# Optimization experiments

Measured on AMD Instinct MI355X. Metric: run time of the kernel, lower is better.

The kernel has to match this reference:

```python
import jax, jax.numpy as jnp
import numpy as np

S, B, D_IN, D_SRC, D_ALIGN = 2048, 64, 512, 512, 512


def setup_inputs() -> dict:
    key = jax.random.key(0)
    ks = jax.random.split(key, 6)
    scale = 0.1  # matches uniform_(-0.1, 0.1) init magnitude
    return {
        "input": jax.random.normal(ks[0], (1, B, D_IN), dtype=jnp.float32),
        "source_hids": jax.random.normal(ks[1], (S, B, D_SRC), dtype=jnp.float32),
        "encoder_padding_mask": jnp.zeros((S, B), dtype=bool),
        "W1": jax.random.uniform(ks[2], (D_ALIGN, D_IN + D_SRC), jnp.float32, -scale, scale),
        "b1": jax.random.uniform(ks[3], (D_ALIGN,), jnp.float32, -scale, scale),
        "W2": jax.random.uniform(ks[4], (1, D_ALIGN), jnp.float32, -scale, scale),
        "b2": jax.random.uniform(ks[5], (1,), jnp.float32, -scale, scale),
    }


def reference(input, source_hids, encoder_padding_mask, W1, b1, W2, b2):
    # input: [1, B, D_in] broadcast over srclen; source_hids: [S, B, D_src]
    s = source_hids.shape[0]
    x = jnp.broadcast_to(input, (s,) + input.shape[1:])          # [S, B, D_in]
    cat = jnp.concatenate((x, source_hids), axis=-1)             # [S, B, D_in+D_src]
    h = jnp.tanh(jnp.einsum('sbd,ad->sba', cat, W1) + b1)        # [S, B, D_align]
    scores = jnp.einsum('sba,oa->sbo', h, W2)[..., 0] + b2[0]    # [S, B]
    scores = jnp.where(encoder_padding_mask, -jnp.inf, scores)
    attn = jax.nn.softmax(scores, axis=0)                        # softmax over srclen
    ctx = jnp.einsum('sb,sbd->bd', attn, source_hids)            # [B, D_src]
    return ctx, attn
```

## Files before the change

### kernel.cpp

```cpp
#include <hip/hip_runtime.h>
#include <hip/hip_bf16.h>
#include <math.h>

#define S_LEN 2048
#define BATCH 64
#define DDIM 512

typedef __attribute__((ext_vector_type(8))) short bf16x8;
typedef __attribute__((ext_vector_type(4))) float f32x4;
typedef __attribute__((ext_vector_type(4))) unsigned int u32x4;

typedef __attribute__((address_space(1))) const void g_void;
typedef __attribute__((address_space(3))) void l_void;

__device__ __forceinline__ unsigned short f2bf(float f) {
  unsigned int u = __float_as_uint(f);
  u += 0x7fffu + ((u >> 16) & 1u);
  return (unsigned short)(u >> 16);
}

__device__ __forceinline__ float tanh_fast(float x) {
  float e = __builtin_amdgcn_exp2f(x * 2.88539008177793f);
  return 1.0f - 2.0f * __builtin_amdgcn_rcpf(e + 1.0f);
}

__global__ __launch_bounds__(256) void prep_kernel(
    const float* __restrict__ W1, const float* __restrict__ b1,
    const float* __restrict__ input, unsigned short* __restrict__ W1b,
    float* __restrict__ uprime) {
  __shared__ float w1row[1024];
  const int a = blockIdx.x;
  const int t = threadIdx.x;
  float4 v = *(const float4*)(W1 + a * 1024 + t * 4);
  *(float4*)(w1row + t * 4) = v;
  if (t >= 128) {
    ushort4 u;
    u.x = f2bf(v.x); u.y = f2bf(v.y); u.z = f2bf(v.z); u.w = f2bf(v.w);
    *(ushort4*)(W1b + a * 512 + (t * 4 - 512)) = u;
  }
  __syncthreads();
  if (t < BATCH) {
    const float4* inp = (const float4*)(input + t * 512);
    const float4* wr = (const float4*)w1row;
    float acc = b1[a];
#pragma unroll 4
    for (int d = 0; d < 128; ++d) {
      float4 x = inp[d], w = wr[d];
      acc += x.x * w.x + x.y * w.y + x.z * w.z + x.w * w.w;
    }
    uprime[t * 512 + a] = acc;
  }
}

__global__ __launch_bounds__(512, 4) void scores_kernel(
    const float* __restrict__ src, const unsigned short* __restrict__ W1b,
    const float* __restrict__ uprime, const float* __restrict__ W2,
    float* __restrict__ scores_t) {
  __shared__ unsigned short A_sm[64 * 64];
  __shared__ unsigned short B_sm[512 * 64];
  __shared__ float s_lds[BATCH];

  const int t = threadIdx.x;
  const int s = blockIdx.x;
  const int w = t >> 6;
  const int lane = t & 63;
  const int quad = lane >> 4;
  const int l15 = lane & 15;

  if (t < BATCH) s_lds[t] = 0.f;

  f32x4 acc[4][4];
#pragma unroll
  for (int i = 0; i < 4; ++i)
#pragma unroll
    for (int j = 0; j < 4; ++j) acc[i][j] = (f32x4){0.f, 0.f, 0.f, 0.f};

  const float* srcblk = src + (size_t)s * (BATCH * DDIM);
  const int ar = t >> 3, ap = t & 7, ac = ap ^ (ar & 7);
  const float* gA = srcblk + ar * DDIM + ac * 8;
  unsigned short* ldsA = A_sm + ar * 64 + ap * 8;
  const int br = lane >> 3, bp = lane & 7, bc = bp ^ (br & 7);
  const unsigned short* gBl = W1b + br * DDIM + bc * 8;

  for (int k0 = 0; k0 < DDIM; k0 += 64) {
#pragma unroll
    for (int g = 0; g < 8; ++g) {
      const unsigned short* gp = gBl + (g * 64 + w * 8) * DDIM + k0;
      unsigned short* lp = B_sm + (g * 64 + w * 8) * 64;
      __builtin_amdgcn_global_load_lds((g_void*)gp, (l_void*)lp, 16, 0, 0);
    }
    {
      const float4 v0 = *(const float4*)(gA + k0);
      const float4 v1 = *(const float4*)(gA + k0 + 4);
      unsigned x0 = __float_as_uint(v0.x) + 0x8000u;
      unsigned y0 = __float_as_uint(v0.y) + 0x8000u;
      unsigned z0 = __float_as_uint(v0.z) + 0x8000u;
      unsigned w0 = __float_as_uint(v0.w) + 0x8000u;
      unsigned x1 = __float_as_uint(v1.x) + 0x8000u;
      unsigned y1 = __float_as_uint(v1.y) + 0x8000u;
      unsigned z1 = __float_as_uint(v1.z) + 0x8000u;
      unsigned w1 = __float_as_uint(v1.w) + 0x8000u;
      u32x4 o;
      o.x = __builtin_amdgcn_perm(y0, x0, 0x07060302u);
      o.y = __builtin_amdgcn_perm(w0, z0, 0x07060302u);
      o.z = __builtin_amdgcn_perm(y1, x1, 0x07060302u);
      o.w = __builtin_amdgcn_perm(w1, z1, 0x07060302u);
      *(u32x4*)ldsA = o;
    }
    __syncthreads();

#pragma unroll
    for (int ks = 0; ks < 2; ++ks) {
      const int c = ks * 4 + quad;
      bf16x8 af[4], bfr[4];
#pragma unroll
      for (int i = 0; i < 4; ++i) {
        const int r = i * 16 + l15;
        af[i] = *(const bf16x8*)(A_sm + r * 64 + ((c ^ (r & 7)) << 3));
      }
#pragma unroll
      for (int j = 0; j < 4; ++j) {
        const int n = w * 64 + j * 16 + l15;
        bfr[j] = *(const bf16x8*)(B_sm + n * 64 + ((c ^ (n & 7)) << 3));
      }
#pragma unroll
      for (int i = 0; i < 4; ++i)
#pragma unroll
        for (int j = 0; j < 4; ++j)
          acc[i][j] = __builtin_amdgcn_mfma_f32_16x16x32_bf16(af[i], bfr[j], acc[i][j], 0, 0, 0);
    }
    __syncthreads();
  }

  float w2r[4];
#pragma unroll
  for (int j = 0; j < 4; ++j) w2r[j] = W2[w * 64 + j * 16 + l15];

#pragma unroll
  for (int i = 0; i < 4; ++i) {
#pragma unroll
    for (int r = 0; r < 4; ++r) {
      const int b = i * 16 + quad * 4 + r;
      const float* up = uprime + b * 512 + w * 64 + l15;
      float sp = 0.f;
#pragma unroll
      for (int j = 0; j < 4; ++j)
        sp += w2r[j] * tanh_fast(acc[i][j][r] + up[j * 16]);
      sp += __shfl_xor(sp, 1);
      sp += __shfl_xor(sp, 2);
      sp += __shfl_xor(sp, 4);
      sp += __shfl_xor(sp, 8);
      if (l15 == 0) atomicAdd(&s_lds[b], sp);
    }
  }
  __syncthreads();
  if (t < BATCH) scores_t[t * S_LEN + s] = s_lds[t];
}

__global__ __launch_bounds__(256) void softmax_kernel(
    const float* __restrict__ scores_t, const unsigned char* __restrict__ mask,
    float* __restrict__ attn_g, float* __restrict__ attn_t, int write_t) {
  __shared__ float red[256];
  const int b = blockIdx.x, t = threadIdx.x;
  float m = -__builtin_inff();
  float sc[8];
#pragma unroll
  for (int c = 0; c < 8; ++c) {
    const int s = t + c * 256;
    sc[c] = mask[s * BATCH + b] ? -__builtin_inff() : scores_t[b * S_LEN + s];
    m = fmaxf(m, sc[c]);
  }
  red[t] = m;
  __syncthreads();
  for (int off = 128; off; off >>= 1) {
    if (t < off) red[t] = fmaxf(red[t], red[t + off]);
    __syncthreads();
  }
  m = red[0];
  __syncthreads();
  float sum = 0.f;
#pragma unroll
  for (int c = 0; c < 8; ++c) sum += __expf(sc[c] - m);
  red[t] = sum;
  __syncthreads();
  for (int off = 128; off; off >>= 1) {
    if (t < off) red[t] += red[t + off];
    __syncthreads();
  }
  const float inv = 1.f / red[0];
#pragma unroll
  for (int c = 0; c < 8; ++c) {
    const int s = t + c * 256;
    const float p = __expf(sc[c] - m) * inv;
    attn_g[s * BATCH + b] = p;
    if (write_t) attn_t[b * S_LEN + s] = p;
  }
}

__global__ __launch_bounds__(256) void ctx_partial_kernel(
    const float* __restrict__ src, const float* __restrict__ attn_t,
    float* __restrict__ partial) {
  __shared__ float a_lds[64];
  const int c = blockIdx.x;
  const int b = blockIdx.y;
  const int t = threadIdx.x;
  if (t < 64) a_lds[t] = attn_t[b * S_LEN + c * 64 + t];
  __syncthreads();
  const int f4i = t & 127;
  const int sh = t >> 7;
  const float4* base =
      (const float4*)src + ((size_t)(c * 64 + sh * 32) * BATCH + b) * 128 + f4i;
  float4 acc = {0.f, 0.f, 0.f, 0.f};
#pragma unroll 8
  for (int i = 0; i < 32; ++i) {
    const float a = a_lds[sh * 32 + i];
    float4 v = base[(size_t)i * BATCH * 128];
    acc.x += a * v.x; acc.y += a * v.y; acc.z += a * v.z; acc.w += a * v.w;
  }
  ((float4*)partial)[((size_t)(c * 2 + sh) * BATCH + b) * 128 + f4i] = acc;
}

__global__ __launch_bounds__(256) void ctx_reduce_kernel(
    const float* __restrict__ partial, float* __restrict__ ctx) {
  const int b = blockIdx.x, t = threadIdx.x;
  const float2* p = (const float2*)partial + (size_t)b * 256 + t;
  float2 acc = {0.f, 0.f};
#pragma unroll 8
  for (int c2 = 0; c2 < 64; ++c2) {
    float2 v = p[(size_t)c2 * BATCH * 256];
    acc.x += v.x; acc.y += v.y;
  }
  ((float2*)ctx)[b * 256 + t] = acc;
}

__global__ __launch_bounds__(256) void ctx_atomic_kernel(
    const float* __restrict__ src, const float* __restrict__ attn_g,
    float* __restrict__ ctx) {
  __shared__ float a_lds[128];
  const int s0 = blockIdx.x * 128, b = blockIdx.y, t = threadIdx.x;
  if (t < 128) a_lds[t] = attn_g[(s0 + t) * BATCH + b];
  __syncthreads();
  const int f4i = t & 127;
  const int sh = t >> 7;
  const float4* base =
      (const float4*)src + ((size_t)(s0 + sh * 64) * BATCH + b) * 128 + f4i;
  float4 acc = {0.f, 0.f, 0.f, 0.f};
#pragma unroll 8
  for (int i = 0; i < 64; ++i) {
    const float a = a_lds[sh * 64 + i];
    float4 v = base[(size_t)i * BATCH * 128];
    acc.x += a * v.x; acc.y += a * v.y; acc.z += a * v.z; acc.w += a * v.w;
  }
  float* cp = ctx + b * DDIM + f4i * 4;
  atomicAdd(cp + 0, acc.x);
  atomicAdd(cp + 1, acc.y);
  atomicAdd(cp + 2, acc.z);
  atomicAdd(cp + 3, acc.w);
}

extern "C" void kernel_launch(void* const* d_in, const int* in_sizes, int n_in,
                              void* d_out, int out_size, void* d_ws, size_t ws_size,
                              hipStream_t stream) {
  const float* input = (const float*)d_in[0];
  const float* src = (const float*)d_in[1];
  const unsigned char* mask = (const unsigned char*)d_in[2];
  const float* W1 = (const float*)d_in[3];
  const float* b1 = (const float*)d_in[4];
  const float* W2 = (const float*)d_in[5];

  float* ctx = (float*)d_out;
  float* attn = (float*)d_out + BATCH * DDIM;

  unsigned short* W1b = (unsigned short*)d_ws;
  float* uprime = (float*)((char*)d_ws + 512 * 1024);
  float* scores_t = (float*)((char*)d_ws + 640 * 1024);
  float* attn_t = (float*)((char*)d_ws + 1152 * 1024);
  float* partial = (float*)((char*)d_ws + 1664 * 1024);
  const size_t NEED_ATTN_T = 1664 * 1024;
  const size_t NEED_PARTIAL = 1664 * 1024 + (size_t)64 * BATCH * DDIM * 4;
  const int have_attn_t = ws_size >= NEED_ATTN_T;
  const int have_partial = ws_size >= NEED_PARTIAL;

  prep_kernel<<<512, 256, 0, stream>>>(W1, b1, input, W1b, uprime);
  scores_kernel<<<S_LEN, 512, 0, stream>>>(src, W1b, uprime, W2, scores_t);
  softmax_kernel<<<BATCH, 256, 0, stream>>>(scores_t, mask, attn, attn_t,
                                            have_attn_t && have_partial);
  if (have_partial) {
    ctx_partial_kernel<<<dim3(32, BATCH), 256, 0, stream>>>(src, attn_t, partial);
    ctx_reduce_kernel<<<BATCH, 256, 0, stream>>>(partial, ctx);
  } else {
    hipMemsetAsync(ctx, 0, BATCH * DDIM * sizeof(float), stream);
    ctx_atomic_kernel<<<dim3(16, BATCH), 256, 0, stream>>>(src, attn, ctx);
  }
}
```

Measured before the change: 494.1 us.

## Process two source positions per block and double-buffer W1 tiles in LDS

New measurement: 505.7 us. +2.3%, slower.

```diff
diff --git a/kernel.cpp b/kernel.cpp
--- a/kernel.cpp
+++ b/kernel.cpp
@@ -22,6 +22,12 @@
 __device__ __forceinline__ float tanh_fast(float x) {
   float e = __builtin_amdgcn_exp2f(x * 2.88539008177793f);
   return 1.0f - 2.0f * __builtin_amdgcn_rcpf(e + 1.0f);
+}
+
+__device__ __forceinline__ unsigned pkbf(float a, float b) {
+  unsigned ua = __float_as_uint(a) + 0x8000u;
+  unsigned ub = __float_as_uint(b) + 0x8000u;
+  return __builtin_amdgcn_perm(ub, ua, 0x07060302u);
 }
 
 __global__ __launch_bounds__(256) void prep_kernel(
@@ -52,84 +58,110 @@
   }
 }
 
-__global__ __launch_bounds__(512, 4) void scores_kernel(
+__global__ __launch_bounds__(512, 2) void scores_kernel(
     const float* __restrict__ src, const unsigned short* __restrict__ W1b,
     const float* __restrict__ uprime, const float* __restrict__ W2,
     float* __restrict__ scores_t) {
-  __shared__ unsigned short A_sm[64 * 64];
-  __shared__ unsigned short B_sm[512 * 64];
-  __shared__ float s_lds[BATCH];
+  __shared__ unsigned short A_sm[128 * 64];
+  __shared__ unsigned short B_sm[2 * 512 * 64];
+  __shared__ float s_lds[128];
 
   const int t = threadIdx.x;
-  const int s = blockIdx.x;
+  const int sblk = blockIdx.x;
   const int w = t >> 6;
   const int lane = t & 63;
   const int quad = lane >> 4;
   const int l15 = lane & 15;
 
-  if (t < BATCH) s_lds[t] = 0.f;
-
-  f32x4 acc[4][4];
-#pragma unroll
-  for (int i = 0; i < 4; ++i)
+  if (t < 128) s_lds[t] = 0.f;
+
+  f32x4 acc[8][4];
+#pragma unroll
+  for (int i = 0; i < 8; ++i)
 #pragma unroll
     for (int j = 0; j < 4; ++j) acc[i][j] = (f32x4){0.f, 0.f, 0.f, 0.f};
 
-  const float* srcblk = src + (size_t)s * (BATCH * DDIM);
-  const int ar = t >> 3, ap = t & 7, ac = ap ^ (ar & 7);
-  const float* gA = srcblk + ar * DDIM + ac * 8;
-  unsigned short* ldsA = A_sm + ar * 64 + ap * 8;
+  const int ar = t >> 2, aq = t & 3;
+  const float* gA = src + (size_t)(sblk * 128) * DDIM + ar * DDIM + aq * 16;
+  const int p0 = (2 * aq) ^ (ar & 7);
+  const int p1 = (2 * aq + 1) ^ (ar & 7);
+  unsigned short* ldsA0 = A_sm + ar * 64 + p0 * 8;
+  unsigned short* ldsA1 = A_sm + ar * 64 + p1 * 8;
+
   const int br = lane >> 3, bp = lane & 7, bc = bp ^ (br & 7);
   const unsigned short* gBl = W1b + br * DDIM + bc * 8;
 
-  for (int k0 = 0; k0 < DDIM; k0 += 64) {
+  {
+    float4 as0 = ((const float4*)gA)[0];
+    float4 as1 = ((const float4*)gA)[1];
+    float4 as2 = ((const float4*)gA)[2];
+    float4 as3 = ((const float4*)gA)[3];
 #pragma unroll
     for (int g = 0; g < 8; ++g) {
-      const unsigned short* gp = gBl + (g * 64 + w * 8) * DDIM + k0;
+      const unsigned short* gp = gBl + (g * 64 + w * 8) * DDIM;
       unsigned short* lp = B_sm + (g * 64 + w * 8) * 64;
       __builtin_amdgcn_global_load_lds((g_void*)gp, (l_void*)lp, 16, 0, 0);
     }
-    {
-      const float4 v0 = *(const float4*)(gA + k0);
-      const float4 v1 = *(const float4*)(gA + k0 + 4);
-      unsigned x0 = __float_as_uint(v0.x) + 0x8000u;
-      unsigned y0 = __float_as_uint(v0.y) + 0x8000u;
-      unsigned z0 = __float_as_uint(v0.z) + 0x8000u;
-      unsigned w0 = __float_as_uint(v0.w) + 0x8000u;
-      unsigned x1 = __float_as_uint(v1.x) + 0x8000u;
-      unsigned y1 = __float_as_uint(v1.y) + 0x8000u;
-      unsigned z1 = __float_as_uint(v1.z) + 0x8000u;
-      unsigned w1 = __float_as_uint(v1.w) + 0x8000u;
-      u32x4 o;
-      o.x = __builtin_amdgcn_perm(y0, x0, 0x07060302u);
-      o.y = __builtin_amdgcn_perm(w0, z0, 0x07060302u);
-      o.z = __builtin_amdgcn_perm(y1, x1, 0x07060302u);
-      o.w = __builtin_amdgcn_perm(w1, z1, 0x07060302u);
-      *(u32x4*)ldsA = o;
-    }
-    __syncthreads();
-
+    u32x4 o0, o1;
+    o0.x = pkbf(as0.x, as0.y); o0.y = pkbf(as0.z, as0.w);
+    o0.z = pkbf(as1.x, as1.y); o0.w = pkbf(as1.z, as1.w);
+    o1.x = pkbf(as2.x, as2.y); o1.y = pkbf(as2.z, as2.w);
+    o1.z = pkbf(as3.x, as3.y); o1.w = pkbf(as3.z, as3.w);
+    *(u32x4*)ldsA0 = o0;
+    *(u32x4*)ldsA1 = o1;
+  }
+  __syncthreads();
+
+  for (int kt = 0; kt < 8; ++kt) {
+    const int cur = kt & 1;
+    const int pf = kt < 7;
+    float4 as0, as1, as2, as3;
+    if (pf) {
+      const float4* gAn = (const float4*)(gA + (kt + 1) * 64);
+      as0 = gAn[0]; as1 = gAn[1]; as2 = gAn[2]; as3 = gAn[3];
+#pragma unroll
+      for (int g = 0; g < 8; ++g) {
+        const unsigned short* gp = gBl + (g * 64 + w * 8) * DDIM + (kt + 1) * 64;
+        unsigned short* lp =
+            B_sm + (cur ^ 1) * (512 * 64) + (g * 64 + w * 8) * 64;
+        __builtin_amdgcn_global_load_lds((g_void*)gp, (l_void*)lp, 16, 0, 0);
+      }
+    }
+
+    const unsigned short* Bc = B_sm + cur * (512 * 64);
 #pragma unroll
     for (int ks = 0; ks < 2; ++ks) {
       const int c = ks * 4 + quad;
-      bf16x8 af[4], bfr[4];
-#pragma unroll
-      for (int i = 0; i < 4; ++i) {
+      bf16x8 af[8], bfr[4];
+#pragma unroll
+      for (int i = 0; i < 8; ++i) {
         const int r = i * 16 + l15;
         af[i] = *(const bf16x8*)(A_sm + r * 64 + ((c ^ (r & 7)) << 3));
       }
 #pragma unroll
       for (int j = 0; j < 4; ++j) {
         const int n = w * 64 + j * 16 + l15;
-        bfr[j] = *(const bf16x8*)(B_sm + n * 64 + ((c ^ (n & 7)) << 3));
+        bfr[j] = *(const bf16x8*)(Bc + n * 64 + ((c ^ (n & 7)) << 3));
       }
 #pragma unroll
-      for (int i = 0; i < 4; ++i)
+      for (int i = 0; i < 8; ++i)
 #pragma unroll
         for (int j = 0; j < 4; ++j)
-          acc[i][j] = __builtin_amdgcn_mfma_f32_16x16x32_bf16(af[i], bfr[j], acc[i][j], 0, 0, 0);
+          acc[i][j] = __builtin_amdgcn_mfma_f32_16x16x32_bf16(af[i], bfr[j],
+                                                              acc[i][j], 0, 0, 0);
     }
     __syncthreads();
+
+    if (pf) {
+      u32x4 o0, o1;
+      o0.x = pkbf(as0.x, as0.y); o0.y = pkbf(as0.z, as0.w);
+      o0.z = pkbf(as1.x, as1.y); o0.w = pkbf(as1.z, as1.w);
+      o1.x = pkbf(as2.x, as2.y); o1.y = pkbf(as2.z, as2.w);
+      o1.z = pkbf(as3.x, as3.y); o1.w = pkbf(as3.z, as3.w);
+      *(u32x4*)ldsA0 = o0;
+      *(u32x4*)ldsA1 = o1;
+    }
+    __syncthreads();
   }
 
   float w2r[4];
@@ -137,10 +169,12 @@
   for (int j = 0; j < 4; ++j) w2r[j] = W2[w * 64 + j * 16 + l15];
 
 #pragma unroll
-  for (int i = 0; i < 4; ++i) {
+  for (int i = 0; i < 8; ++i) {
 #pragma unroll
     for (int r = 0; r < 4; ++r) {
-      const int b = i * 16 + quad * 4 + r;
+      const int row = i * 16 + quad * 4 + r;
+      const int b = row & 63;
+      const int sl = row >> 6;
       const float* up = uprime + b * 512 + w * 64 + l15;
       float sp = 0.f;
 #pragma unroll
@@ -150,11 +184,12 @@
       sp += __shfl_xor(sp, 2);
       sp += __shfl_xor(sp, 4);
       sp += __shfl_xor(sp, 8);
-      if (l15 == 0) atomicAdd(&s_lds[b], sp);
-    }
-  }
-  __syncthreads();
-  if (t < BATCH) scores_t[t * S_LEN + s] = s_lds[t];
+      if (l15 == 0) atomicAdd(&s_lds[sl * 64 + b], sp);
+    }
+  }
+  __syncthreads();
+  if (t < 128)
+    scores_t[(t & 63) * S_LEN + sblk * 2 + (t >> 6)] = s_lds[t];
 }
 
 __global__ __launch_bounds__(256) void softmax_kernel(
@@ -282,7 +317,7 @@
   const int have_partial = ws_size >= NEED_PARTIAL;
 
   prep_kernel<<<512, 256, 0, stream>>>(W1, b1, input, W1b, uprime);
-  scores_kernel<<<S_LEN, 512, 0, stream>>>(src, W1b, uprime, W2, scores_t);
+  scores_kernel<<<S_LEN / 2, 512, 0, stream>>>(src, W1b, uprime, W2, scores_t);
   softmax_kernel<<<BATCH, 256, 0, stream>>>(scores_t, mask, attn, attn_t,
                                             have_attn_t && have_partial);
   if (have_partial) {
```

## Stage whole src slab in LDS and stream W1 fragments directly from global

Applied to the files above, without the earlier changes.

Measured after the change: 506.0 us. +2.4%, slower.

```diff
diff --git a/kernel.cpp b/kernel.cpp
--- a/kernel.cpp
+++ b/kernel.cpp
@@ -9,9 +9,6 @@
 typedef __attribute__((ext_vector_type(8))) short bf16x8;
 typedef __attribute__((ext_vector_type(4))) float f32x4;
 typedef __attribute__((ext_vector_type(4))) unsigned int u32x4;
-
-typedef __attribute__((address_space(1))) const void g_void;
-typedef __attribute__((address_space(3))) void l_void;
 
 __device__ __forceinline__ unsigned short f2bf(float f) {
   unsigned int u = __float_as_uint(f);
@@ -24,9 +21,15 @@
   return 1.0f - 2.0f * __builtin_amdgcn_rcpf(e + 1.0f);
 }
 
+__device__ __forceinline__ unsigned pkbf(float a, float b) {
+  unsigned ua = __float_as_uint(a) + 0x8000u;
+  unsigned ub = __float_as_uint(b) + 0x8000u;
+  return __builtin_amdgcn_perm(ub, ua, 0x07060302u);
+}
+
 __global__ __launch_bounds__(256) void prep_kernel(
     const float* __restrict__ W1, const float* __restrict__ b1,
-    const float* __restrict__ input, unsigned short* __restrict__ W1b,
+    const float* __restrict__ input, unsigned short* __restrict__ W1bT,
     float* __restrict__ uprime) {
   __shared__ float w1row[1024];
   const int a = blockIdx.x;
@@ -36,7 +39,10 @@
   if (t >= 128) {
     ushort4 u;
     u.x = f2bf(v.x); u.y = f2bf(v.y); u.z = f2bf(v.z); u.w = f2bf(v.w);
-    *(ushort4*)(W1b + a * 512 + (t * 4 - 512)) = u;
+    const int d = t * 4 - 512;
+    const int kc = d >> 3;
+    const int e = d & 7;
+    *(ushort4*)(W1bT + ((size_t)kc * 512 + a) * 8 + e) = u;
   }
   __syncthreads();
   if (t < BATCH) {
@@ -52,12 +58,11 @@
   }
 }
 
-__global__ __launch_bounds__(512, 4) void scores_kernel(
-    const float* __restrict__ src, const unsigned short* __restrict__ W1b,
+__global__ __launch_bounds__(256, 2) void scores_kernel(
+    const float* __restrict__ src, const unsigned short* __restrict__ W1bT,
     const float* __restrict__ uprime, const float* __restrict__ W2,
     float* __restrict__ scores_t) {
-  __shared__ unsigned short A_sm[64 * 64];
-  __shared__ unsigned short B_sm[512 * 64];
+  __shared__ unsigned short A_sm[64 * 512];
   __shared__ float s_lds[BATCH];
 
   const int t = threadIdx.x;
@@ -69,82 +74,65 @@
 
   if (t < BATCH) s_lds[t] = 0.f;
 
-  f32x4 acc[4][4];
+  f32x4 acc[4][8];
 #pragma unroll
   for (int i = 0; i < 4; ++i)
 #pragma unroll
-    for (int j = 0; j < 4; ++j) acc[i][j] = (f32x4){0.f, 0.f, 0.f, 0.f};
-
-  const float* srcblk = src + (size_t)s * (BATCH * DDIM);
-  const int ar = t >> 3, ap = t & 7, ac = ap ^ (ar & 7);
-  const float* gA = srcblk + ar * DDIM + ac * 8;
-  unsigned short* ldsA = A_sm + ar * 64 + ap * 8;
-  const int br = lane >> 3, bp = lane & 7, bc = bp ^ (br & 7);
-  const unsigned short* gBl = W1b + br * DDIM + bc * 8;
-
-  for (int k0 = 0; k0 < DDIM; k0 += 64) {
-#pragma unroll
-    for (int g = 0; g < 8; ++g) {
-      const unsigned short* gp = gBl + (g * 64 + w * 8) * DDIM + k0;
-      unsigned short* lp = B_sm + (g * 64 + w * 8) * 64;
-      __builtin_amdgcn_global_load_lds((g_void*)gp, (l_void*)lp, 16, 0, 0);
-    }
-    {
-      const float4 v0 = *(const float4*)(gA + k0);
-      const float4 v1 = *(const float4*)(gA + k0 + 4);
-      unsigned x0 = __float_as_uint(v0.x) + 0x8000u;
-      unsigned y0 = __float_as_uint(v0.y) + 0x8000u;
-      unsigned z0 = __float_as_uint(v0.z) + 0x8000u;
-      unsigned w0 = __float_as_uint(v0.w) + 0x8000u;
-      unsigned x1 = __float_as_uint(v1.x) + 0x8000u;
-      unsigned y1 = __float_as_uint(v1.y) + 0x8000u;
-      unsigned z1 = __float_as_uint(v1.z) + 0x8000u;
-      unsigned w1 = __float_as_uint(v1.w) + 0x8000u;
+    for (int j = 0; j < 8; ++j) acc[i][j] = (f32x4){0.f, 0.f, 0.f, 0.f};
+
+  {
+    const float4* gsrc = (const float4*)(src + (size_t)s * (BATCH * DDIM));
+    const int cc = t & 63;
+#pragma unroll 4
+    for (int n = 0; n < 16; ++n) {
+      const int row = n * 4 + (t >> 6);
+      const float4 v0 = gsrc[row * 128 + cc * 2];
+      const float4 v1 = gsrc[row * 128 + cc * 2 + 1];
       u32x4 o;
-      o.x = __builtin_amdgcn_perm(y0, x0, 0x07060302u);
-      o.y = __builtin_amdgcn_perm(w0, z0, 0x07060302u);
-      o.z = __builtin_amdgcn_perm(y1, x1, 0x07060302u);
-      o.w = __builtin_amdgcn_perm(w1, z1, 0x07060302u);
-      *(u32x4*)ldsA = o;
-    }
-    __syncthreads();
-
-#pragma unroll
-    for (int ks = 0; ks < 2; ++ks) {
-      const int c = ks * 4 + quad;
-      bf16x8 af[4], bfr[4];
-#pragma unroll
-      for (int i = 0; i < 4; ++i) {
-        const int r = i * 16 + l15;
-        af[i] = *(const bf16x8*)(A_sm + r * 64 + ((c ^ (r & 7)) << 3));
-      }
-#pragma unroll
-      for (int j = 0; j < 4; ++j) {
-        const int n = w * 64 + j * 16 + l15;
-        bfr[j] = *(const bf16x8*)(B_sm + n * 64 + ((c ^ (n & 7)) << 3));
-      }
-#pragma unroll
-      for (int i = 0; i < 4; ++i)
-#pragma unroll
-        for (int j = 0; j < 4; ++j)
-          acc[i][j] = __builtin_amdgcn_mfma_f32_16x16x32_bf16(af[i], bfr[j], acc[i][j], 0, 0, 0);
-    }
-    __syncthreads();
-  }
-
-  float w2r[4];
-#pragma unroll
-  for (int j = 0; j < 4; ++j) w2r[j] = W2[w * 64 + j * 16 + l15];
+      o.x = pkbf(v0.x, v0.y);
+      o.y = pkbf(v0.z, v0.w);
+      o.z = pkbf(v1.x, v1.y);
+      o.w = pkbf(v1.z, v1.w);
+      const int p = cc ^ (row & 7);
+      *(u32x4*)(A_sm + row * 512 + p * 8) = o;
+    }
+  }
+  __syncthreads();
+
+  const unsigned short* gB = W1bT + ((size_t)quad * 512 + w * 128 + l15) * 8;
+#pragma unroll 4
+  for (int n = 0; n < 16; ++n) {
+    bf16x8 bb[8], af[4];
+#pragma unroll
+    for (int j = 0; j < 8; ++j)
+      bb[j] = *(const bf16x8*)(gB + ((size_t)n * 4 * 512 + j * 16) * 8);
+    const int c = n * 4 + quad;
+#pragma unroll
+    for (int i = 0; i < 4; ++i) {
+      const int r = i * 16 + l15;
+      af[i] = *(const bf16x8*)(A_sm + r * 512 + ((c ^ (r & 7)) << 3));
+    }
+#pragma unroll
+    for (int i = 0; i < 4; ++i)
+#pragma unroll
+      for (int j = 0; j < 8; ++j)
+        acc[i][j] = __builtin_amdgcn_mfma_f32_16x16x32_bf16(af[i], bb[j],
+                                                            acc[i][j], 0, 0, 0);
+  }
+
+  float w2r[8];
+#pragma unroll
+  for (int j = 0; j < 8; ++j) w2r[j] = W2[w * 128 + j * 16 + l15];
 
 #pragma unroll
   for (int i = 0; i < 4; ++i) {
 #pragma unroll
     for (int r = 0; r < 4; ++r) {
       const int b = i * 16 + quad * 4 + r;
-      const float* up = uprime + b * 512 + w * 64 + l15;
+      const float* up = uprime + b * 512 + w * 128 + l15;
       float sp = 0.f;
 #pragma unroll
-      for (int j = 0; j < 4; ++j)
+      for (int j = 0; j < 8; ++j)
         sp += w2r[j] * tanh_fast(acc[i][j][r] + up[j * 16]);
       sp += __shfl_xor(sp, 1);
       sp += __shfl_xor(sp, 2);
@@ -271,7 +259,7 @@
   float* ctx = (float*)d_out;
   float* attn = (float*)d_out + BATCH * DDIM;
 
-  unsigned short* W1b = (unsigned short*)d_ws;
+  unsigned short* W1bT = (unsigned short*)d_ws;
   float* uprime = (float*)((char*)d_ws + 512 * 1024);
   float* scores_t = (float*)((char*)d_ws + 640 * 1024);
   float* attn_t = (float*)((char*)d_ws + 1152 * 1024);
@@ -281,8 +269,8 @@
   const int have_attn_t = ws_size >= NEED_ATTN_T;
   const int have_partial = ws_size >= NEED_PARTIAL;
 
-  prep_kernel<<<512, 256, 0, stream>>>(W1, b1, input, W1b, uprime);
-  scores_kernel<<<S_LEN, 512, 0, stream>>>(src, W1b, uprime, W2, scores_t);
+  prep_kernel<<<512, 256, 0, stream>>>(W1, b1, input, W1bT, uprime);
+  scores_kernel<<<S_LEN, 256, 0, stream>>>(src, W1bT, uprime, W2, scores_t);
   softmax_kernel<<<BATCH, 256, 0, stream>>>(scores_t, mask, attn, attn_t,
                                             have_attn_t && have_partial);
   if (have_partial) {
```
